# Optimization experiments

Hardware: AMD Instinct MI355X
Metric: run time of the kernel (lower is better)

## Reference

```python
import jax, jax.numpy as jnp
import numpy as np

# dims / hyperparams (match init_kwargs)
B, C, H, W = 1, 48, 160, 160
COUT = 48
RANK = 12
K = 8          # topK neighbors
WS = 32        # window_size
KS = 3         # local conv kernel / local mask size
M = 3          # circ_rows
DELTA = 10.0
LEAK = 0.01


def circ_dense(x, w, m):
    """CircDense: x (N, Cin), w (Cout//m, 1, Cin) -> (N, Cout).
    Equivalent to circular-pad + conv1d in the torch module."""
    cin = x.shape[1]
    xp = jnp.concatenate([x, x[:, : m - 1]], axis=1)            # circular pad to Cin+m-1
    xw = jnp.stack([xp[:, j : j + cin] for j in range(m)], 1)   # (N, m, Cin)
    out = jnp.einsum('njc,ic->nij', xw, w[:, 0, :])             # (N, Cout//m, m)
    return out.reshape(x.shape[0], -1)


def windowed_topk(h, k, ws, ks):
    """knn.windowedTopK: per 32x32 window, K nearest neighbors by feature L2,
    excluding the ks x ks local neighborhood (localMask). Returns (B,K,H,W)
    global flat pixel indices."""
    b, c, hh, ww = h.shape
    nh, nw = hh // ws, ww // ws
    ws2 = ws * ws
    hw = h.reshape(b, c, nh, ws, nw, ws).transpose(0, 2, 4, 3, 5, 1)
    hw = hw.reshape(b, nh, nw, ws2, c)                          # windowed features
    sq = jnp.sum(hw * hw, -1)
    d = sq[..., :, None] + sq[..., None, :] - 2.0 * jnp.einsum('bijnc,bijmc->bijnm', hw, hw)
    r = jnp.arange(ws2) // ws
    cc = jnp.arange(ws2) % ws
    loc = (jnp.abs(r[:, None] - r[None, :]) <= ks // 2) & (jnp.abs(cc[:, None] - cc[None, :]) <= ks // 2)
    d = jnp.where(loc, 1e10, d)                                 # mask local neighborhood
    _, idx = jax.lax.top_k(-d, k)                               # (b,nh,nw,ws2,k) local idx
    wi = jnp.arange(nh)[:, None, None, None]
    wj = jnp.arange(nw)[None, :, None, None]
    g = (wi * ws + idx // ws) * ww + (wj * ws + idx % ws)       # global flat idx
    g = g.reshape(b, nh, nw, ws, ws, k).transpose(0, 5, 1, 3, 2, 4).reshape(b, k, hh, ww)
    return g


def low_rank_ecc(h, edge, W0, b0, WL, WR, Wk, bk):
    b, k, hh, ww = edge.shape
    n = hh * ww
    cin = h.shape[1]
    hf = h.reshape(b, cin, n)
    ef = edge.reshape(b, k, n)
    # gather neighbor (vertex) features: (b, cin, k, n) -> (b, k, n, cin)
    vertex = jax.vmap(lambda hb, eb: hb[:, eb])(hf, ef).transpose(0, 2, 3, 1)
    center = hf.transpose(0, 2, 1)[:, None]                     # (b,1,n,cin)
    label = vertex - center                                     # edge labels
    lt = label.reshape(-1, cin)                                 # (B0, Cin), B0=b*k*n
    vt = vertex.reshape(-1, cin)
    theta = jax.nn.leaky_relu(lt @ W0.T + b0, LEAK)
    tL = circ_dense(theta, WL, M).reshape(-1, COUT, RANK)       # (B0, Cout, rank)
    tR = circ_dense(theta, WR, M).reshape(-1, cin, RANK)        # (B0, Cin, rank)
    kap = theta @ Wk.T + bk                                     # (B0, rank)
    tmp = kap * jnp.einsum('bcr,bc->br', tR, vt)                # thetaR^T @ v, scaled
    out = jnp.einsum('bor,br->bo', tL, tmp)                     # thetaL @ (...)
    gamma = jnp.exp(-jnp.sum(lt * lt, 1, keepdims=True) / DELTA)
    out = (gamma * out).reshape(b, k, n, COUT).mean(1)          # mean over K neighbors
    return out.transpose(0, 2, 1).reshape(b, COUT, hh, ww)


def local_conv(h, w):
    p = KS // 2
    hp = jnp.pad(h, ((0, 0), (0, 0), (p, p), (p, p)), mode='reflect')
    return jax.lax.conv_general_dilated(hp, w, (1, 1), 'VALID',
                                        dimension_numbers=('NCHW', 'OIHW', 'NCHW'))


def setup_inputs() -> dict:
    key = jax.random.key(0)
    ks_ = jax.random.split(key, 9)
    s_in = 1.0 / np.sqrt(C)
    return {
        'h': jax.random.normal(ks_[0], (B, C, H, W), jnp.float32),
        'W0': jax.random.normal(ks_[1], (C, C), jnp.float32) * s_in,
        'b0': jnp.zeros((C,), jnp.float32),
        'WL': jax.random.normal(ks_[2], (RANK * COUT // M, 1, C), jnp.float32) * s_in,
        'WR': jax.random.normal(ks_[3], (RANK * C // M, 1, C), jnp.float32) * s_in,
        'Wk': jax.random.normal(ks_[4], (RANK, C), jnp.float32) * s_in,
        'bk': jnp.zeros((RANK,), jnp.float32),
        'Wconv': jax.random.normal(ks_[5], (COUT, C, KS, KS), jnp.float32) * (1.0 / np.sqrt(C * KS * KS)),
        'bias': jnp.zeros((1, COUT, 1, 1), jnp.float32),
    }


def reference(h, W0, b0, WL, WR, Wk, bk, Wconv, bias):
    edge = windowed_topk(h, K, WS, KS)
    hNL = low_rank_ecc(h, edge, W0, b0, WL, WR, Wk, bk)
    hL = local_conv(h, Wconv)
    return (hNL + hL) / 2.0 + bias
```

## Files before the change

kernel.cpp:

```cpp
#include <hip/hip_runtime.h>

#define CC    48
#define HH    160
#define WWID  160
#define NPIX  25600
#define KK    8

typedef unsigned short u16;
typedef unsigned int u32;
typedef __attribute__((ext_vector_type(8))) short bf16x8;
typedef __attribute__((ext_vector_type(4))) float f32x4;

__device__ __forceinline__ float bf2f(u16 u) {
    return __uint_as_float(((unsigned int)u) << 16);
}
__device__ __forceinline__ u16 f2bf(float f) {
    unsigned int x = __float_as_uint(f);
    return (u16)((x + 0x7FFFu + ((x >> 16) & 1u)) >> 16);
}

#define OFF_B0    0
#define OFF_BK    48
#define OFF_WKT   60
#define OFF_WBH   636
#define OFF_WBL   8828
#define OFF_WLH   17020
#define OFF_WLL   21628
#define OFF_SQP   26236
#define OFF_W0V   51836
#define OFF_VTB   1280636
#define OFF_HHT   3738236
#define OFF_HLT   4557436
#define OFF_PARTK 5376636

__global__ void prep_kernel(const float* W0, const float* b0, const float* WL,
                            const float* WR, const float* Wk, const float* bk,
                            float* ws) {
    float* b0f = ws + OFF_B0;
    float* bkf = ws + OFF_BK;
    float* wkt = ws + OFF_WKT;
    u16*   wbh = (u16*)(ws + OFF_WBH);
    u16*   wbl = (u16*)(ws + OFF_WBL);
    u16*   wlh = (u16*)(ws + OFF_WLH);
    u16*   wll = (u16*)(ws + OFF_WLL);
    int t = blockIdx.x * 256 + threadIdx.x;
    int stride = gridDim.x * 256;
    for (int i = t; i < 16384; i += stride) {
        int col = i >> 6, k = i & 63;
        float v = 0.f;
        if (k < 48) {
            if (col < 192)      v = WR[(4*k + (col & 3))*48 + (col >> 2)];
            else if (col < 240) v = W0[(col - 192)*48 + k];
        }
        u16 hi = f2bf(v);
        wbh[i] = hi;
        wbl[i] = f2bf(v - bf2f(hi));
    }
    for (int i = t; i < 9216; i += stride) {
        int o = i / 192, k = i % 192;
        float v = WL[(4*o + (k & 3))*48 + (k >> 2)];
        u16 hi = f2bf(v);
        wlh[i] = hi;
        wll[i] = f2bf(v - bf2f(hi));
    }
    for (int i = t; i < 576; i += stride) { int c = i / 12, r = i % 12; wkt[i] = Wk[r*48 + c]; }
    for (int i = t; i < 48; i += stride) { b0f[i] = b0[i]; }
    for (int i = t; i < 12; i += stride) { bkf[i] = bk[i]; }
}

__global__ __launch_bounds__(256) void split_kernel(const float* h, float* sqp,
                                                    u16* hht, u16* hlt) {
    int tid = threadIdx.x;
    int p = blockIdx.x * 128 + (tid >> 1);
    int half = tid & 1;
    float sq = 0.f;
    u16 hh[24], hl[24];
    #pragma unroll
    for (int i = 0; i < 24; i++) {
        int c = half*24 + i;
        float v = h[c*NPIX + p];
        sq = fmaf(v, v, sq);
        u16 hi = f2bf(v);
        hh[i] = hi;
        hl[i] = f2bf(v - bf2f(hi));
    }
    sq += __shfl_xor(sq, 1, 64);
    if (half == 0) sqp[p] = sq;
    uint4* dh = (uint4*)&hht[(long)p*64 + half*24];
    uint4* dl = (uint4*)&hlt[(long)p*64 + half*24];
    const uint4* s1 = (const uint4*)hh;
    const uint4* s2 = (const uint4*)hl;
    dh[0] = s1[0]; dh[1] = s1[1]; dh[2] = s1[2];
    dl[0] = s2[0]; dl[1] = s2[1]; dl[2] = s2[2];
    if (half) {
        uint4 z = make_uint4(0, 0, 0, 0);
        uint4* zh = (uint4*)&hht[(long)p*64 + 48];
        uint4* zl = (uint4*)&hlt[(long)p*64 + 48];
        zh[0] = z; zh[1] = z;
        zl[0] = z; zl[1] = z;
    }
}

__global__ __launch_bounds__(512) void pixvt_mfma(const u16* hht, const u16* hlt,
                                                  const float* ws, float* w0v, u16* vtb) {
    __shared__ __align__(16) char smem[38912];
    u16*   a_hi = (u16*)smem;
    u16*   a_lo = (u16*)(smem + 8192);
    u16*   vt_s = (u16*)smem;
    float* w0_s = (float*)(smem + 25600);

    const u16* wbh = (const u16*)(ws + OFF_WBH);
    const u16* wbl = (const u16*)(ws + OFF_WBL);

    int tid = threadIdx.x;
    int pbase = blockIdx.x * 64;

    {
        int blk = tid >> 6, row = tid & 63;
        int swz = (blk ^ (row & 7)) * 8;
        *(uint4*)&a_hi[row*64 + swz] = *(const uint4*)&hht[(long)(pbase + row)*64 + blk*8];
        *(uint4*)&a_lo[row*64 + swz] = *(const uint4*)&hlt[(long)(pbase + row)*64 + blk*8];
    }
    __syncthreads();

    int w = tid >> 6, lane = tid & 63;
    int lm = lane & 15, lg = lane >> 4;
    int c2a = 2*w, c2b = 2*w + 1;

    f32x4 acc0[4], acc1[4];
    #pragma unroll
    for (int t = 0; t < 4; t++) { acc0[t] = (f32x4){0.f,0.f,0.f,0.f}; acc1[t] = (f32x4){0.f,0.f,0.f,0.f}; }

    #pragma unroll
    for (int s = 0; s < 2; s++) {
        int lblk = 4*s + lg;
        int aswz = (lblk ^ (lm & 7)) * 8;
        bf16x8 ah0 = *(const bf16x8*)&a_hi[( 0 + lm)*64 + aswz];
        bf16x8 ah1 = *(const bf16x8*)&a_hi[(16 + lm)*64 + aswz];
        bf16x8 ah2 = *(const bf16x8*)&a_hi[(32 + lm)*64 + aswz];
        bf16x8 ah3 = *(const bf16x8*)&a_hi[(48 + lm)*64 + aswz];
        bf16x8 al0 = *(const bf16x8*)&a_lo[( 0 + lm)*64 + aswz];
        bf16x8 al1 = *(const bf16x8*)&a_lo[(16 + lm)*64 + aswz];
        bf16x8 al2 = *(const bf16x8*)&a_lo[(32 + lm)*64 + aswz];
        bf16x8 al3 = *(const bf16x8*)&a_lo[(48 + lm)*64 + aswz];
        {
            int col = c2a*16 + lm;
            bf16x8 bh = *(const bf16x8*)&wbh[col*64 + lblk*8];
            bf16x8 bl = *(const bf16x8*)&wbl[col*64 + lblk*8];
            acc0[0] = __builtin_amdgcn_mfma_f32_16x16x32_bf16(ah0, bh, acc0[0], 0, 0, 0);
            acc0[0] = __builtin_amdgcn_mfma_f32_16x16x32_bf16(ah0, bl, acc0[0], 0, 0, 0);
            acc0[0] = __builtin_amdgcn_mfma_f32_16x16x32_bf16(al0, bh, acc0[0], 0, 0, 0);
            acc0[1] = __builtin_amdgcn_mfma_f32_16x16x32_bf16(ah1, bh, acc0[1], 0, 0, 0);
            acc0[1] = __builtin_amdgcn_mfma_f32_16x16x32_bf16(ah1, bl, acc0[1], 0, 0, 0);
            acc0[1] = __builtin_amdgcn_mfma_f32_16x16x32_bf16(al1, bh, acc0[1], 0, 0, 0);
            acc0[2] = __builtin_amdgcn_mfma_f32_16x16x32_bf16(ah2, bh, acc0[2], 0, 0, 0);
            acc0[2] = __builtin_amdgcn_mfma_f32_16x16x32_bf16(ah2, bl, acc0[2], 0, 0, 0);
            acc0[2] = __builtin_amdgcn_mfma_f32_16x16x32_bf16(al2, bh, acc0[2], 0, 0, 0);
            acc0[3] = __builtin_amdgcn_mfma_f32_16x16x32_bf16(ah3, bh, acc0[3], 0, 0, 0);
            acc0[3] = __builtin_amdgcn_mfma_f32_16x16x32_bf16(ah3, bl, acc0[3], 0, 0, 0);
            acc0[3] = __builtin_amdgcn_mfma_f32_16x16x32_bf16(al3, bh, acc0[3], 0, 0, 0);
        }
        if (c2b < 15) {
            int col = c2b*16 + lm;
            bf16x8 bh = *(const bf16x8*)&wbh[col*64 + lblk*8];
            bf16x8 bl = *(const bf16x8*)&wbl[col*64 + lblk*8];
            acc1[0] = __builtin_amdgcn_mfma_f32_16x16x32_bf16(ah0, bh, acc1[0], 0, 0, 0);
            acc1[0] = __builtin_amdgcn_mfma_f32_16x16x32_bf16(ah0, bl, acc1[0], 0, 0, 0);
            acc1[0] = __builtin_amdgcn_mfma_f32_16x16x32_bf16(al0, bh, acc1[0], 0, 0, 0);
            acc1[1] = __builtin_amdgcn_mfma_f32_16x16x32_bf16(ah1, bh, acc1[1], 0, 0, 0);
            acc1[1] = __builtin_amdgcn_mfma_f32_16x16x32_bf16(ah1, bl, acc1[1], 0, 0, 0);
            acc1[1] = __builtin_amdgcn_mfma_f32_16x16x32_bf16(al1, bh, acc1[1], 0, 0, 0);
            acc1[2] = __builtin_amdgcn_mfma_f32_16x16x32_bf16(ah2, bh, acc1[2], 0, 0, 0);
            acc1[2] = __builtin_amdgcn_mfma_f32_16x16x32_bf16(ah2, bl, acc1[2], 0, 0, 0);
            acc1[2] = __builtin_amdgcn_mfma_f32_16x16x32_bf16(al2, bh, acc1[2], 0, 0, 0);
            acc1[3] = __builtin_amdgcn_mfma_f32_16x16x32_bf16(ah3, bh, acc1[3], 0, 0, 0);
            acc1[3] = __builtin_amdgcn_mfma_f32_16x16x32_bf16(ah3, bl, acc1[3], 0, 0, 0);
            acc1[3] = __builtin_amdgcn_mfma_f32_16x16x32_bf16(al3, bh, acc1[3], 0, 0, 0);
        }
    }
    __syncthreads();

    {
        int col = c2a*16 + lm;
        if (c2a < 12) {
            #pragma unroll
            for (int t = 0; t < 4; t++)
                #pragma unroll
                for (int r = 0; r < 4; r++)
                    vt_s[(t*16 + lg*4 + r)*200 + col] = f2bf(acc0[t][r]);
        } else {
            int o = col - 192;
            #pragma unroll
            for (int t = 0; t < 4; t++)
                #pragma unroll
                for (int r = 0; r < 4; r++)
                    w0_s[(t*16 + lg*4 + r)*52 + o] = acc0[t][r];
        }
    }
    if (c2b < 15) {
        int col = c2b*16 + lm;
        if (c2b < 12) {
            #pragma unroll
            for (int t = 0; t < 4; t++)
                #pragma unroll
                for (int r = 0; r < 4; r++)
                    vt_s[(t*16 + lg*4 + r)*200 + col] = f2bf(acc1[t][r]);
        } else {
            int o = col - 192;
            #pragma unroll
            for (int t = 0; t < 4; t++)
                #pragma unroll
                for (int r = 0; r < 4; r++)
                    w0_s[(t*16 + lg*4 + r)*52 + o] = acc1[t][r];
        }
    }
    __syncthreads();

    {
        int px = tid >> 3, c8 = tid & 7;
        #pragma unroll
        for (int j = 0; j < 3; j++) {
            int ch = c8 + 8*j;
            uint4 v = *(const uint4*)&vt_s[px*200 + ch*8];
            *(uint4*)&vtb[(long)(pbase + px)*192 + ch*8] = v;
        }
        float* dst = w0v + (long)(pbase + px)*48 + c8*6;
        const float* src = w0_s + px*52 + c8*6;
        #pragma unroll
        for (int k = 0; k < 3; k++) {
            float2 v2 = *(const float2*)&src[k*2];
            *(float2*)&dst[k*2] = v2;
        }
    }
}

__global__ __launch_bounds__(512, 8) void topk_mfma(const u16* hht, const u16* hlt,
                                                    const float* sqp, u32* partk) {
    __shared__ u16 ca_hi[128*64];
    __shared__ u16 ca_lo[128*64];
    __shared__ float sq_s[128];

    int tid = threadIdx.x;
    int b = (blockIdx.x & 7) * 200 + (blockIdx.x >> 3);
    int chunk = b & 7, pg = (b >> 3) & 7, win = b >> 6;
    int wi = win / 5, wj = win % 5;
    int base = wi*32*WWID + wj*32;

    #pragma unroll
    for (int r = 0; r < 2; r++) {
        int task = r*512 + tid;
        int blk = task >> 7, row = task & 127;
        int swz = (blk ^ (row & 7)) * 8;
        int ml = chunk*128 + row;
        long gp = base + (ml>>5)*WWID + (ml&31);
        *(uint4*)&ca_hi[row*64 + swz] = *(const uint4*)&hht[gp*64 + blk*8];
        *(uint4*)&ca_lo[row*64 + swz] = *(const uint4*)&hlt[gp*64 + blk*8];
    }
    if (tid < 128) {
        int ml = chunk*128 + tid;
        sq_s[tid] = sqp[base + (ml>>5)*WWID + (ml&31)];
    }
    __syncthreads();

    int w = tid >> 6, lane = tid & 63;
    int lm = lane & 15, lg = lane >> 4;

    int nl = pg*128 + w*16 + lm;
    long gpx = base + (nl>>5)*WWID + (nl&31);

    f32x4 acc[8];
    #pragma unroll
    for (int t = 0; t < 8; t++) acc[t] = (f32x4){0.f, 0.f, 0.f, 0.f};

    #pragma unroll
    for (int s = 0; s < 2; s++) {
        int lblk = 4*s + lg;
        int ko = lblk * 8;
        bf16x8 bh = *(const bf16x8*)&hht[gpx*64 + ko];
        bf16x8 bl = *(const bf16x8*)&hlt[gpx*64 + ko];
        #pragma unroll
        for (int t = 0; t < 8; t++) {
            int aoff = (t*16 + lm)*64 + (lblk ^ (lm & 7))*8;
            bf16x8 ah = *(const bf16x8*)&ca_hi[aoff];
            bf16x8 al = *(const bf16x8*)&ca_lo[aoff];
            acc[t] = __builtin_amdgcn_mfma_f32_16x16x32_bf16(ah, bh, acc[t], 0, 0, 0);
            acc[t] = __builtin_amdgcn_mfma_f32_16x16x32_bf16(ah, bl, acc[t], 0, 0, 0);
            acc[t] = __builtin_amdgcn_mfma_f32_16x16x32_bf16(al, bh, acc[t], 0, 0, 0);
        }
    }

    int rn = nl >> 5, cn = nl & 31;
    int rowok[8], colok[8];
    #pragma unroll
    for (int t = 0; t < 8; t++) {
        int rm = chunk*4 + (t >> 1);
        int dr = rn - rm; dr = dr < 0 ? -dr : dr;
        rowok[t] = (dr <= 1);
    }
    #pragma unroll
    for (int j = 0; j < 8; j++) {
        int cm = (j >> 2)*16 + lg*4 + (j & 3);
        int dc = cn - cm; dc = dc < 0 ? -dc : dc;
        colok[j] = (dc <= 1);
    }

    u32 k8[8];
    #pragma unroll
    for (int s = 0; s < 8; s++) k8[s] = 0xFFFFFFFFu;

    #pragma unroll
    for (int t = 0; t < 8; t++) {
        #pragma unroll
        for (int r = 0; r < 4; r++) {
            int cl = t*16 + lg*4 + r;
            int ml = chunk*128 + cl;
            float d = fmaf(-2.0f, acc[t][r], sq_s[cl]);
            u32 u = __float_as_uint(d);
            u32 key = u ^ (0x80000000u | (u32)((int)u >> 31));
            key = (key & 0xFFFFFC00u) | (u32)ml;
            bool bad = rowok[t] && colok[(t & 1)*4 + r];
            key = bad ? 0xFFFFFFFFu : key;
            #pragma unroll
            for (int s = 0; s < 8; s++) {
                u32 lo = min(k8[s], key);
                u32 hi = max(k8[s], key);
                k8[s] = lo; key = hi;
            }
        }
    }

    #pragma unroll
    for (int st = 0; st < 2; st++) {
        int mk = (st == 0) ? 16 : 32;
        u32 o[8];
        #pragma unroll
        for (int s = 0; s < 8; s++) o[s] = (u32)__shfl_xor((int)k8[s], mk, 64);
        u32 c0 = min(k8[0], o[7]);
        u32 c1 = min(k8[1], o[6]);
        u32 c2 = min(k8[2], o[5]);
        u32 c3 = min(k8[3], o[4]);
        u32 c4 = min(k8[4], o[3]);
        u32 c5 = min(k8[5], o[2]);
        u32 c6 = min(k8[6], o[1]);
        u32 c7 = min(k8[7], o[0]);
        u32 a, bb;
        a = min(c0,c4); bb = max(c0,c4); c0 = a; c4 = bb;
        a = min(c1,c5); bb = max(c1,c5); c1 = a; c5 = bb;
        a = min(c2,c6); bb = max(c2,c6); c2 = a; c6 = bb;
        a = min(c3,c7); bb = max(c3,c7); c3 = a; c7 = bb;
        a = min(c0,c2); bb = max(c0,c2); c0 = a; c2 = bb;
        a = min(c1,c3); bb = max(c1,c3); c1 = a; c3 = bb;
        a = min(c4,c6); bb = max(c4,c6); c4 = a; c6 = bb;
        a = min(c5,c7); bb = max(c5,c7); c5 = a; c7 = bb;
        a = min(c0,c1); bb = max(c0,c1); c0 = a; c1 = bb;
        a = min(c2,c3); bb = max(c2,c3); c2 = a; c3 = bb;
        a = min(c4,c5); bb = max(c4,c5); c4 = a; c5 = bb;
        a = min(c6,c7); bb = max(c6,c7); c6 = a; c7 = bb;
        k8[0]=c0; k8[1]=c1; k8[2]=c2; k8[3]=c3; k8[4]=c4; k8[5]=c5; k8[6]=c6; k8[7]=c7;
    }

    {
        int n = base + (nl >> 5)*WWID + (nl & 31);
        u32 v0, v1;
        if      (lg == 0) { v0 = k8[0]; v1 = k8[1]; }
        else if (lg == 1) { v0 = k8[2]; v1 = k8[3]; }
        else if (lg == 2) { v0 = k8[4]; v1 = k8[5]; }
        else              { v0 = k8[6]; v1 = k8[7]; }
        u32* pk = partk + (long)chunk*8*NPIX + (long)(2*lg)*NPIX + n;
        pk[0]    = v0;
        pk[NPIX] = v1;
    }
}

__global__ __launch_bounds__(128, 4) void ecc_kernel(const float* ws, const u32* partk,
                                                     const u16* vtb, float* outp) {
    const float* b0f = ws + OFF_B0;
    const float* bkf = ws + OFF_BK;
    const float* wkt = ws + OFF_WKT;
    const float* w0v = ws + OFF_W0V;
    const float* sqp = ws + OFF_SQP;
    const u16*   wlh = (const u16*)(ws + OFF_WLH);
    const u16*   wll = (const u16*)(ws + OFF_WLL);

    __shared__ u16 th_s[128][50];
    __shared__ __align__(16) u16 ub_s[16*200];

    int tid = threadIdx.x;
    int sb = (blockIdx.x & 7) * 200 + (blockIdx.x >> 3);
    int pix = tid >> 3, sh = tid & 7;
    int n = sb * 16 + pix;

    u32 k8[8];
    {
        const u32* pk = partk + (long)sh*8*NPIX + n;
        #pragma unroll
        for (int s = 0; s < 8; s++) k8[s] = pk[(long)s*NPIX];
    }
    #pragma unroll
    for (int st = 0; st < 3; st++) {
        int mk = 1 << st;
        u32 o[8];
        #pragma unroll
        for (int s = 0; s < 8; s++) o[s] = (u32)__shfl_xor((int)k8[s], mk, 64);
        u32 c0 = min(k8[0], o[7]);
        u32 c1 = min(k8[1], o[6]);
        u32 c2 = min(k8[2], o[5]);
        u32 c3 = min(k8[3], o[4]);
        u32 c4 = min(k8[4], o[3]);
        u32 c5 = min(k8[5], o[2]);
        u32 c6 = min(k8[6], o[1]);
        u32 c7 = min(k8[7], o[0]);
        u32 a, bb;
        a = min(c0,c4); bb = max(c0,c4); c0 = a; c4 = bb;
        a = min(c1,c5); bb = max(c1,c5); c1 = a; c5 = bb;
        a = min(c2,c6); bb = max(c2,c6); c2 = a; c6 = bb;
        a = min(c3,c7); bb = max(c3,c7); c3 = a; c7 = bb;
        a = min(c0,c2); bb = max(c0,c2); c0 = a; c2 = bb;
        a = min(c1,c3); bb = max(c1,c3); c1 = a; c3 = bb;
        a = min(c4,c6); bb = max(c4,c6); c4 = a; c6 = bb;
        a = min(c5,c7); bb = max(c5,c7); c5 = a; c7 = bb;
        a = min(c0,c1); bb = max(c0,c1); c0 = a; c1 = bb;
        a = min(c2,c3); bb = max(c2,c3); c2 = a; c3 = bb;
        a = min(c4,c5); bb = max(c4,c5); c4 = a; c5 = bb;
        a = min(c6,c7); bb = max(c6,c7); c6 = a; c7 = bb;
        k8[0]=c0; k8[1]=c1; k8[2]=c2; k8[3]=c3; k8[4]=c4; k8[5]=c5; k8[6]=c6; k8[7]=c7;
    }
    u32 key;
    {
        u32 m0 = (sh & 1) ? k8[1] : k8[0];
        u32 m1 = (sh & 1) ? k8[3] : k8[2];
        u32 m2 = (sh & 1) ? k8[5] : k8[4];
        u32 m3 = (sh & 1) ? k8[7] : k8[6];
        u32 n0 = (sh & 2) ? m1 : m0;
        u32 n1 = (sh & 2) ? m3 : m2;
        key = (sh & 4) ? n1 : n0;
    }
    int ml = (int)(key & 1023u);
    u32 uf = key & 0xFFFFFC00u;
    u32 uu = (uf & 0x80000000u) ? (uf ^ 0x80000000u) : ~uf;
    float d = __uint_as_float(uu);
    int y = n / WWID, x = n % WWID;
    int wy = (y >> 5) << 5, wx = (x >> 5) << 5;
    int m = (wy + (ml >> 5)) * WWID + (wx + (ml & 31));
    float gamma = expf(-(d + sqp[n]) * 0.1f);

    const u16* vrow = vtb + (long)m * 192;
    uint4 vv[8];
    #pragma unroll
    for (int jj = 0; jj < 8; jj++) vv[jj] = *(const uint4*)&vrow[jj*8];

    float th[48];
    {
        const float4* wm4 = (const float4*)(w0v + (long)m * 48);
        const float4* wn4 = (const float4*)(w0v + (long)n * 48);
        #pragma unroll
        for (int i = 0; i < 12; i++) {
            float4 a = wm4[i];
            float4 b = wn4[i];
            float x0 = a.x - b.x + b0f[4*i+0];
            float x1 = a.y - b.y + b0f[4*i+1];
            float x2 = a.z - b.z + b0f[4*i+2];
            float x3 = a.w - b.w + b0f[4*i+3];
            th[4*i+0] = (x0 >= 0.f) ? x0 : 0.01f * x0;
            th[4*i+1] = (x1 >= 0.f) ? x1 : 0.01f * x1;
            th[4*i+2] = (x2 >= 0.f) ? x2 : 0.01f * x2;
            th[4*i+3] = (x3 >= 0.f) ? x3 : 0.01f * x3;
        }
    }

    #pragma unroll
    for (int i = 0; i < 24; i++) {
        ushort2 pr;
        pr.x = f2bf(th[2*i]);
        pr.y = f2bf(th[2*i+1]);
        *(ushort2*)&th_s[tid][2*i] = pr;
    }

    float kap[12];
    #pragma unroll
    for (int r = 0; r < 12; r++) kap[r] = bkf[r];
    #pragma unroll
    for (int c = 0; c < 48; c++) {
        float t = th[c];
        const float* wkc = wkt + c*12;
        #pragma unroll
        for (int r = 0; r < 12; r++) kap[r] = fmaf(wkc[r], t, kap[r]);
    }

    float sr[12];
    #pragma unroll
    for (int r = 0; r < 12; r++) sr[r] = 0.f;
    #pragma unroll
    for (int ch = 0; ch < 3; ch++) {
        if (ch > 0) {
            #pragma unroll
            for (int jj = 0; jj < 8; jj++) vv[jj] = *(const uint4*)&vrow[(ch*8 + jj)*8];
        }
        #pragma unroll
        for (int jj = 0; jj < 8; jj++) {
            int j = ch*8 + jj;
            uint4 v4 = vv[jj];
            #pragma unroll
            for (int half = 0; half < 2; half++) {
                int cp = 2*j + half;
                u32 w0_ = half ? v4.z : v4.x;
                u32 w1_ = half ? v4.w : v4.y;
                float vx = bf2f((u16)(w0_ & 0xffff));
                float vy = bf2f((u16)(w0_ >> 16));
                float vz = bf2f((u16)(w1_ & 0xffff));
                float vw = bf2f((u16)(w1_ >> 16));
                int i1 = (cp + 1 < 48) ? cp + 1 : cp - 47;
                int i2 = (cp + 2 < 48) ? cp + 2 : cp - 46;
                float t0 = th[cp], t1 = th[i1], t2 = th[i2];
                sr[0] = fmaf(t0, vx, sr[0]); sr[1]  = fmaf(t1, vx, sr[1]);  sr[2]  = fmaf(t2, vx, sr[2]);
                sr[3] = fmaf(t0, vy, sr[3]); sr[4]  = fmaf(t1, vy, sr[4]);  sr[5]  = fmaf(t2, vy, sr[5]);
                sr[6] = fmaf(t0, vz, sr[6]); sr[7]  = fmaf(t1, vz, sr[7]);  sr[8]  = fmaf(t2, vz, sr[8]);
                sr[9] = fmaf(t0, vw, sr[9]); sr[10] = fmaf(t1, vw, sr[10]); sr[11] = fmaf(t2, vw, sr[11]);
            }
        }
    }

    float tmp[12];
    #pragma unroll
    for (int r = 0; r < 12; r++) tmp[r] = kap[r] * sr[r];

    __syncthreads();

    float acc0[6], acc1[6], acc2[6], acc3[6];
    #pragma unroll
    for (int j = 0; j < 6; j++) { acc0[j] = 0.f; acc1[j] = 0.f; acc2[j] = 0.f; acc3[j] = 0.f; }
    #pragma unroll 1
    for (int e = 0; e < 8; e++) {
        int srcl = (tid & 56) + e;
        int row  = (tid & 120) + e;
        float tm[12];
        #pragma unroll
        for (int r = 0; r < 12; r++) tm[r] = __shfl(tmp[r], srcl, 64);
        float ge = __shfl(gamma, srcl, 64);
        #pragma unroll
        for (int j = 0; j < 6; j++) {
            int cp = sh + 8*j;
            int i1 = (cp + 1 < 48) ? cp + 1 : cp - 47;
            int i2 = (cp + 2 < 48) ? cp + 2 : cp - 46;
            float t0 = bf2f(th_s[row][cp]);
            float t1 = bf2f(th_s[row][i1]);
            float t2 = bf2f(th_s[row][i2]);
            float u0 = tm[0]*t0 + tm[1]*t1 + tm[2]*t2;
            float u1 = tm[3]*t0 + tm[4]*t1 + tm[5]*t2;
            float u2 = tm[6]*t0 + tm[7]*t1 + tm[8]*t2;
            float u3 = tm[9]*t0 + tm[10]*t1 + tm[11]*t2;
            acc0[j] = fmaf(ge, u0, acc0[j]);
            acc1[j] = fmaf(ge, u1, acc1[j]);
            acc2[j] = fmaf(ge, u2, acc2[j]);
            acc3[j] = fmaf(ge, u3, acc3[j]);
        }
    }
    {
        u16* ub = &ub_s[pix*200];
        #pragma unroll
        for (int j = 0; j < 6; j++) {
            int cp = sh + 8*j;
            ushort4 st;
            st.x = f2bf(acc0[j]); st.y = f2bf(acc1[j]);
            st.z = f2bf(acc2[j]); st.w = f2bf(acc3[j]);
            *(ushort4*)&ub[cp*4] = st;
        }
    }
    __syncthreads();

    {
        int w2 = tid >> 6;
        int lane = tid & 63;
        int lm = lane & 15, lg = lane >> 4;
        int nb = sb * 16;
        if (w2 == 0) {
            f32x4 a0 = (f32x4){0.f,0.f,0.f,0.f};
            f32x4 a1 = (f32x4){0.f,0.f,0.f,0.f};
            #pragma unroll
            for (int ks = 0; ks < 6; ks++) {
                bf16x8 a = *(const bf16x8*)&ub_s[lm*200 + ks*32 + lg*8];
                bf16x8 bh0 = *(const bf16x8*)&wlh[( 0 + lm)*192 + ks*32 + lg*8];
                bf16x8 bl0 = *(const bf16x8*)&wll[( 0 + lm)*192 + ks*32 + lg*8];
                bf16x8 bh1 = *(const bf16x8*)&wlh[(16 + lm)*192 + ks*32 + lg*8];
                bf16x8 bl1 = *(const bf16x8*)&wll[(16 + lm)*192 + ks*32 + lg*8];
                a0 = __builtin_amdgcn_mfma_f32_16x16x32_bf16(a, bh0, a0, 0, 0, 0);
                a0 = __builtin_amdgcn_mfma_f32_16x16x32_bf16(a, bl0, a0, 0, 0, 0);
                a1 = __builtin_amdgcn_mfma_f32_16x16x32_bf16(a, bh1, a1, 0, 0, 0);
                a1 = __builtin_amdgcn_mfma_f32_16x16x32_bf16(a, bl1, a1, 0, 0, 0);
            }
            #pragma unroll
            for (int r = 0; r < 4; r++) {
                int px = lg*4 + r;
                outp[(long)( 0 + lm)*NPIX + nb + px] = 0.0625f * a0[r];
                outp[(long)(16 + lm)*NPIX + nb + px] = 0.0625f * a1[r];
            }
        } else {
            f32x4 a2 = (f32x4){0.f,0.f,0.f,0.f};
            #pragma unroll
            for (int ks = 0; ks < 6; ks++) {
                bf16x8 a = *(const bf16x8*)&ub_s[lm*200 + ks*32 + lg*8];
                bf16x8 bh2 = *(const bf16x8*)&wlh[(32 + lm)*192 + ks*32 + lg*8];
                bf16x8 bl2 = *(const bf16x8*)&wll[(32 + lm)*192 + ks*32 + lg*8];
                a2 = __builtin_amdgcn_mfma_f32_16x16x32_bf16(a, bh2, a2, 0, 0, 0);
                a2 = __builtin_amdgcn_mfma_f32_16x16x32_bf16(a, bl2, a2, 0, 0, 0);
            }
            #pragma unroll
            for (int r = 0; r < 4; r++) {
                int px = lg*4 + r;
                outp[(long)(32 + lm)*NPIX + nb + px] = 0.0625f * a2[r];
            }
        }
    }
}

#define OCH 4
__global__ __launch_bounds__(320) void conv_kernel(const float* h, const float* wc,
                                                   const float* bias, float* outp) {
    int sb = (blockIdx.x & 7) * 120 + (blockIdx.x >> 3);
    int og = sb % 12;
    int yp = sb / 12;
    int t  = threadIdx.x;
    int ty = t / 160;
    int x  = t % 160;
    int y  = yp * 2 + ty;

    int idx9[9];
    #pragma unroll
    for (int dy = 0; dy < 3; dy++) {
        int yy = y + dy - 1;
        yy = yy < 0 ? -yy : (yy >= HH ? 2*HH - 2 - yy : yy);
        #pragma unroll
        for (int dx = 0; dx < 3; dx++) {
            int xx = x + dx - 1;
            xx = xx < 0 ? -xx : (xx >= WWID ? 2*WWID - 2 - xx : xx);
            idx9[dy*3 + dx] = yy * WWID + xx;
        }
    }

    float acc[OCH];
    #pragma unroll
    for (int oi = 0; oi < OCH; oi++) acc[oi] = 0.f;

    const float* wbase = wc + og * OCH * 432;
    for (int c = 0; c < 48; c++) {
        float v[9];
        #pragma unroll
        for (int k = 0; k < 9; k++) v[k] = h[c*NPIX + idx9[k]];
        #pragma unroll
        for (int oi = 0; oi < OCH; oi++) {
            const float* w9 = wbase + oi*432 + c*9;
            float a = acc[oi];
            a = fmaf(v[0], w9[0], a);
            a = fmaf(v[1], w9[1], a);
            a = fmaf(v[2], w9[2], a);
            a = fmaf(v[3], w9[3], a);
            a = fmaf(v[4], w9[4], a);
            a = fmaf(v[5], w9[5], a);
            a = fmaf(v[6], w9[6], a);
            a = fmaf(v[7], w9[7], a);
            a = fmaf(v[8], w9[8], a);
            acc[oi] = a;
        }
    }

    int p = y * WWID + x;
    #pragma unroll
    for (int oi = 0; oi < OCH; oi++) {
        int o = og * OCH + oi;
        outp[o*NPIX + p] = outp[o*NPIX + p] + 0.5f * acc[oi] + bias[o];
    }
}

extern "C" void kernel_launch(void* const* d_in, const int* in_sizes, int n_in,
                              void* d_out, int out_size, void* d_ws, size_t ws_size,
                              hipStream_t stream) {
    const float* h    = (const float*)d_in[0];
    const float* W0   = (const float*)d_in[1];
    const float* b0   = (const float*)d_in[2];
    const float* WL   = (const float*)d_in[3];
    const float* WR   = (const float*)d_in[4];
    const float* Wk   = (const float*)d_in[5];
    const float* bk   = (const float*)d_in[6];
    const float* Wc   = (const float*)d_in[7];
    const float* bias = (const float*)d_in[8];

    float* ws     = (float*)d_ws;
    float* sqp    = ws + OFF_SQP;
    float* w0v    = ws + OFF_W0V;
    u16*   vtb    = (u16*)(ws + OFF_VTB);
    u16*   hht    = (u16*)(ws + OFF_HHT);
    u16*   hlt    = (u16*)(ws + OFF_HLT);
    u32*   partk  = (u32*)(ws + OFF_PARTK);
    float* outp   = (float*)d_out;

    prep_kernel<<<dim3(16), dim3(256), 0, stream>>>(W0, b0, WL, WR, Wk, bk, ws);
    split_kernel<<<dim3(200), dim3(256), 0, stream>>>(h, sqp, hht, hlt);
    topk_mfma<<<dim3(1600), dim3(512), 0, stream>>>(hht, hlt, sqp, partk);
    pixvt_mfma<<<dim3(400), dim3(512), 0, stream>>>(hht, hlt, ws, w0v, vtb);
    ecc_kernel<<<dim3(1600), dim3(128), 0, stream>>>(ws, partk, vtb, outp);
    conv_kernel<<<dim3(960), dim3(320), 0, stream>>>(h, Wc, bias, outp);
}
```

Baseline: 132.2 us.

## Split each neighbor's channel work across two lanes in ECC kernel

Doubles the ECC block to 256 threads so each (pixel, neighbor) pair is handled by two lanes, each covering half of the 48 channels. The kap and sr reductions are combined with xor-shuffles, and the top-k merge now uses shuffle strides that skip the idle half-lane. The accumulation loop and the final MFMA stage are redistributed so three waves each compute one 16-row output tile instead of two waves with uneven work. The aim is lower register pressure and more latency hiding per pixel, at the cost of extra shuffles and duplicated top-k merging.

```diff
diff --git a/kernel.cpp b/kernel.cpp
--- a/kernel.cpp
+++ b/kernel.cpp
@@ -372,8 +372,8 @@
     }
 }
 
-__global__ __launch_bounds__(128, 4) void ecc_kernel(const float* ws, const u32* partk,
-                                                     const u16* vtb, float* outp) {
+__global__ __launch_bounds__(256) void ecc_kernel(const float* ws, const u32* partk,
+                                                  const u16* vtb, float* outp) {
     const float* b0f = ws + OFF_B0;
     const float* bkf = ws + OFF_BK;
     const float* wkt = ws + OFF_WKT;
@@ -387,18 +387,26 @@
 
     int tid = threadIdx.x;
     int sb = (blockIdx.x & 7) * 200 + (blockIdx.x >> 3);
-    int pix = tid >> 3, sh = tid & 7;
+    int pix = tid >> 4;
+    int lane16 = tid & 15;
+    int ek = lane16 >> 1;
+    int half = lane16 & 1;
+    int lane = tid & 63;
+    int erow = tid >> 1;
     int n = sb * 16 + pix;
 
     u32 k8[8];
-    {
-        const u32* pk = partk + (long)sh*8*NPIX + n;
+    if (half == 0) {
+        const u32* pk = partk + (long)ek*8*NPIX + n;
         #pragma unroll
         for (int s = 0; s < 8; s++) k8[s] = pk[(long)s*NPIX];
+    } else {
+        #pragma unroll
+        for (int s = 0; s < 8; s++) k8[s] = 0xFFFFFFFFu;
     }
     #pragma unroll
     for (int st = 0; st < 3; st++) {
-        int mk = 1 << st;
+        int mk = 2 << st;
         u32 o[8];
         #pragma unroll
         for (int s = 0; s < 8; s++) o[s] = (u32)__shfl_xor((int)k8[s], mk, 64);
@@ -425,16 +433,25 @@
         a = min(c6,c7); bb = max(c6,c7); c6 = a; c7 = bb;
         k8[0]=c0; k8[1]=c1; k8[2]=c2; k8[3]=c3; k8[4]=c4; k8[5]=c5; k8[6]=c6; k8[7]=c7;
     }
-    u32 key;
+    u32 muxval;
     {
-        u32 m0 = (sh & 1) ? k8[1] : k8[0];
-        u32 m1 = (sh & 1) ? k8[3] : k8[2];
-        u32 m2 = (sh & 1) ? k8[5] : k8[4];
-        u32 m3 = (sh & 1) ? k8[7] : k8[6];
-        u32 n0 = (sh & 2) ? m1 : m0;
-        u32 n1 = (sh & 2) ? m3 : m2;
-        key = (sh & 4) ? n1 : n0;
-    }
+        int sc = ek;
+        u32 m0 = (sc & 1) ? k8[1] : k8[0];
+        u32 m1 = (sc & 1) ? k8[3] : k8[2];
+        u32 m2 = (sc & 1) ? k8[5] : k8[4];
+        u32 m3 = (sc & 2) ? ((sc & 1) ? k8[3] : k8[2]) : m0;
+        u32 n0 = (sc & 2) ? m1 : m0;
+        u32 n1 = (sc & 2) ? ((sc & 1) ? k8[7] : k8[6]) : m2;
+        u32 q0 = (sc & 1) ? k8[1] : k8[0];
+        u32 q1 = (sc & 1) ? k8[3] : k8[2];
+        u32 q2 = (sc & 1) ? k8[5] : k8[4];
+        u32 q3 = (sc & 1) ? k8[7] : k8[6];
+        u32 r0 = (sc & 2) ? q1 : q0;
+        u32 r1 = (sc & 2) ? q3 : q2;
+        muxval = (sc & 4) ? r1 : r0;
+        (void)m3; (void)n0; (void)n1;
+    }
+    u32 key = (u32)__shfl((int)muxval, (lane & 48) + 2*ek, 64);
     int ml = (int)(key & 1023u);
     u32 uf = key & 0xFFFFFC00u;
     u32 uu = (uf & 0x80000000u) ? (uf ^ 0x80000000u) : ~uf;
@@ -444,81 +461,100 @@
     int m = (wy + (ml >> 5)) * WWID + (wx + (ml & 31));
     float gamma = expf(-(d + sqp[n]) * 0.1f);
 
-    const u16* vrow = vtb + (long)m * 192;
-    uint4 vv[8];
-    #pragma unroll
-    for (int jj = 0; jj < 8; jj++) vv[jj] = *(const uint4*)&vrow[jj*8];
-
-    float th[48];
+    const u16* vrow = vtb + (long)m * 192 + half*96;
+    uint4 vv[6];
+    #pragma unroll
+    for (int jj = 0; jj < 6; jj++) vv[jj] = *(const uint4*)&vrow[jj*8];
+
+    float th26[26];
     {
-        const float4* wm4 = (const float4*)(w0v + (long)m * 48);
-        const float4* wn4 = (const float4*)(w0v + (long)n * 48);
-        #pragma unroll
-        for (int i = 0; i < 12; i++) {
+        const float4* wm4 = (const float4*)(w0v + (long)m * 48) + half*6;
+        const float4* wn4 = (const float4*)(w0v + (long)n * 48) + half*6;
+        #pragma unroll
+        for (int i = 0; i < 6; i++) {
             float4 a = wm4[i];
             float4 b = wn4[i];
-            float x0 = a.x - b.x + b0f[4*i+0];
-            float x1 = a.y - b.y + b0f[4*i+1];
-            float x2 = a.z - b.z + b0f[4*i+2];
-            float x3 = a.w - b.w + b0f[4*i+3];
-            th[4*i+0] = (x0 >= 0.f) ? x0 : 0.01f * x0;
-            th[4*i+1] = (x1 >= 0.f) ? x1 : 0.01f * x1;
-            th[4*i+2] = (x2 >= 0.f) ? x2 : 0.01f * x2;
-            th[4*i+3] = (x3 >= 0.f) ? x3 : 0.01f * x3;
-        }
-    }
-
+            int c0 = half*24 + 4*i;
+            float x0 = a.x - b.x + b0f[c0+0];
+            float x1 = a.y - b.y + b0f[c0+1];
+            float x2 = a.z - b.z + b0f[c0+2];
+            float x3 = a.w - b.w + b0f[c0+3];
+            th26[4*i+0] = (x0 >= 0.f) ? x0 : 0.01f * x0;
+            th26[4*i+1] = (x1 >= 0.f) ? x1 : 0.01f * x1;
+            th26[4*i+2] = (x2 >= 0.f) ? x2 : 0.01f * x2;
+            th26[4*i+3] = (x3 >= 0.f) ? x3 : 0.01f * x3;
+        }
+    }
+    th26[24] = __shfl_xor(th26[0], 1, 64);
+    th26[25] = __shfl_xor(th26[1], 1, 64);
+
+    #pragma unroll
+    for (int i = 0; i < 12; i++) {
+        ushort2 pr;
+        pr.x = f2bf(th26[2*i]);
+        pr.y = f2bf(th26[2*i+1]);
+        *(ushort2*)&th_s[erow][half*24 + 2*i] = pr;
+    }
+
+    float kap[12];
+    #pragma unroll
+    for (int r = 0; r < 12; r++) kap[r] = half ? 0.f : bkf[r];
     #pragma unroll
     for (int i = 0; i < 24; i++) {
-        ushort2 pr;
-        pr.x = f2bf(th[2*i]);
-        pr.y = f2bf(th[2*i+1]);
-        *(ushort2*)&th_s[tid][2*i] = pr;
-    }
-
-    float kap[12];
-    #pragma unroll
-    for (int r = 0; r < 12; r++) kap[r] = bkf[r];
-    #pragma unroll
-    for (int c = 0; c < 48; c++) {
-        float t = th[c];
+        int c = half*24 + i;
+        float t = th26[i];
         const float* wkc = wkt + c*12;
         #pragma unroll
         for (int r = 0; r < 12; r++) kap[r] = fmaf(wkc[r], t, kap[r]);
     }
+    #pragma unroll
+    for (int r = 0; r < 12; r++) kap[r] += __shfl_xor(kap[r], 1, 64);
 
     float sr[12];
     #pragma unroll
     for (int r = 0; r < 12; r++) sr[r] = 0.f;
     #pragma unroll
-    for (int ch = 0; ch < 3; ch++) {
-        if (ch > 0) {
-            #pragma unroll
-            for (int jj = 0; jj < 8; jj++) vv[jj] = *(const uint4*)&vrow[(ch*8 + jj)*8];
-        }
-        #pragma unroll
-        for (int jj = 0; jj < 8; jj++) {
-            int j = ch*8 + jj;
-            uint4 v4 = vv[jj];
-            #pragma unroll
-            for (int half = 0; half < 2; half++) {
-                int cp = 2*j + half;
-                u32 w0_ = half ? v4.z : v4.x;
-                u32 w1_ = half ? v4.w : v4.y;
-                float vx = bf2f((u16)(w0_ & 0xffff));
-                float vy = bf2f((u16)(w0_ >> 16));
-                float vz = bf2f((u16)(w1_ & 0xffff));
-                float vw = bf2f((u16)(w1_ >> 16));
-                int i1 = (cp + 1 < 48) ? cp + 1 : cp - 47;
-                int i2 = (cp + 2 < 48) ? cp + 2 : cp - 46;
-                float t0 = th[cp], t1 = th[i1], t2 = th[i2];
-                sr[0] = fmaf(t0, vx, sr[0]); sr[1]  = fmaf(t1, vx, sr[1]);  sr[2]  = fmaf(t2, vx, sr[2]);
-                sr[3] = fmaf(t0, vy, sr[3]); sr[4]  = fmaf(t1, vy, sr[4]);  sr[5]  = fmaf(t2, vy, sr[5]);
-                sr[6] = fmaf(t0, vz, sr[6]); sr[7]  = fmaf(t1, vz, sr[7]);  sr[8]  = fmaf(t2, vz, sr[8]);
-                sr[9] = fmaf(t0, vw, sr[9]); sr[10] = fmaf(t1, vw, sr[10]); sr[11] = fmaf(t2, vw, sr[11]);
-            }
-        }
-    }
+    for (int j = 0; j < 6; j++) {
+        uint4 v4 = vv[j];
+        #pragma unroll
+        for (int hf = 0; hf < 2; hf++) {
+            int l = 2*j + hf;
+            u32 w0_ = hf ? v4.z : v4.x;
+            u32 w1_ = hf ? v4.w : v4.y;
+            float vx = bf2f((u16)(w0_ & 0xffff));
+            float vy = bf2f((u16)(w0_ >> 16));
+            float vz = bf2f((u16)(w1_ & 0xffff));
+            float vw = bf2f((u16)(w1_ >> 16));
+            float t0 = th26[l], t1 = th26[l+1], t2 = th26[l+2];
+            sr[0] = fmaf(t0, vx, sr[0]); sr[1]  = fmaf(t1, vx, sr[1]);  sr[2]  = fmaf(t2, vx, sr[2]);
+            sr[3] = fmaf(t0, vy, sr[3]); sr[4]  = fmaf(t1, vy, sr[4]);  sr[5]  = fmaf(t2, vy, sr[5]);
+            sr[6] = fmaf(t0, vz, sr[6]); sr[7]  = fmaf(t1, vz, sr[7]);  sr[8]  = fmaf(t2, vz, sr[8]);
+            sr[9] = fmaf(t0, vw, sr[9]); sr[10] = fmaf(t1, vw, sr[10]); sr[11] = fmaf(t2, vw, sr[11]);
+        }
+    }
+    #pragma unroll
+    for (int jj = 0; jj < 6; jj++) vv[jj] = *(const uint4*)&vrow[(6 + jj)*8];
+    #pragma unroll
+    for (int j = 0; j < 6; j++) {
+        uint4 v4 = vv[j];
+        #pragma unroll
+        for (int hf = 0; hf < 2; hf++) {
+            int l = 12 + 2*j + hf;
+            u32 w0_ = hf ? v4.z : v4.x;
+            u32 w1_ = hf ? v4.w : v4.y;
+            float vx = bf2f((u16)(w0_ & 0xffff));
+            float vy = bf2f((u16)(w0_ >> 16));
+            float vz = bf2f((u16)(w1_ & 0xffff));
+            float vw = bf2f((u16)(w1_ >> 16));
+            float t0 = th26[l], t1 = th26[l+1], t2 = th26[l+2];
+            sr[0] = fmaf(t0, vx, sr[0]); sr[1]  = fmaf(t1, vx, sr[1]);  sr[2]  = fmaf(t2, vx, sr[2]);
+            sr[3] = fmaf(t0, vy, sr[3]); sr[4]  = fmaf(t1, vy, sr[4]);  sr[5]  = fmaf(t2, vy, sr[5]);
+            sr[6] = fmaf(t0, vz, sr[6]); sr[7]  = fmaf(t1, vz, sr[7]);  sr[8]  = fmaf(t2, vz, sr[8]);
+            sr[9] = fmaf(t0, vw, sr[9]); sr[10] = fmaf(t1, vw, sr[10]); sr[11] = fmaf(t2, vw, sr[11]);
+        }
+    }
+    #pragma unroll
+    for (int r = 0; r < 12; r++) sr[r] += __shfl_xor(sr[r], 1, 64);
 
     float tmp[12];
     #pragma unroll
@@ -526,20 +562,20 @@
 
     __syncthreads();
 
-    float acc0[6], acc1[6], acc2[6], acc3[6];
-    #pragma unroll
-    for (int j = 0; j < 6; j++) { acc0[j] = 0.f; acc1[j] = 0.f; acc2[j] = 0.f; acc3[j] = 0.f; }
+    float acc0[3], acc1[3], acc2[3], acc3[3];
+    #pragma unroll
+    for (int j = 0; j < 3; j++) { acc0[j] = 0.f; acc1[j] = 0.f; acc2[j] = 0.f; acc3[j] = 0.f; }
     #pragma unroll 1
     for (int e = 0; e < 8; e++) {
-        int srcl = (tid & 56) + e;
-        int row  = (tid & 120) + e;
+        int srcl = (lane & 48) + 2*e;
+        int row  = pix*8 + e;
         float tm[12];
         #pragma unroll
         for (int r = 0; r < 12; r++) tm[r] = __shfl(tmp[r], srcl, 64);
         float ge = __shfl(gamma, srcl, 64);
         #pragma unroll
-        for (int j = 0; j < 6; j++) {
-            int cp = sh + 8*j;
+        for (int j = 0; j < 3; j++) {
+            int cp = lane16 + 16*j;
             int i1 = (cp + 1 < 48) ? cp + 1 : cp - 47;
             int i2 = (cp + 2 < 48) ? cp + 2 : cp - 46;
             float t0 = bf2f(th_s[row][cp]);
@@ -558,8 +594,8 @@
     {
         u16* ub = &ub_s[pix*200];
         #pragma unroll
-        for (int j = 0; j < 6; j++) {
-            int cp = sh + 8*j;
+        for (int j = 0; j < 3; j++) {
+            int cp = lane16 + 16*j;
             ushort4 st;
             st.x = f2bf(acc0[j]); st.y = f2bf(acc1[j]);
             st.z = f2bf(acc2[j]); st.w = f2bf(acc3[j]);
@@ -570,44 +606,22 @@
 
     {
         int w2 = tid >> 6;
-        int lane = tid & 63;
-        int lm = lane & 15, lg = lane >> 4;
-        int nb = sb * 16;
-        if (w2 == 0) {
+        if (w2 < 3) {
+            int lm = lane & 15, lg = lane >> 4;
+            int nb = sb * 16;
             f32x4 a0 = (f32x4){0.f,0.f,0.f,0.f};
-            f32x4 a1 = (f32x4){0.f,0.f,0.f,0.f};
             #pragma unroll
             for (int ks = 0; ks < 6; ks++) {
                 bf16x8 a = *(const bf16x8*)&ub_s[lm*200 + ks*32 + lg*8];
-                bf16x8 bh0 = *(const bf16x8*)&wlh[( 0 + lm)*192 + ks*32 + lg*8];
-                bf16x8 bl0 = *(const bf16x8*)&wll[( 0 + lm)*192 + ks*32 + lg*8];
-                bf16x8 bh1 = *(const bf16x8*)&wlh[(16 + lm)*192 + ks*32 + lg*8];
-                bf16x8 bl1 = *(const bf16x8*)&wll[(16 + lm)*192 + ks*32 + lg*8];
-                a0 = __builtin_amdgcn_mfma_f32_16x16x32_bf16(a, bh0, a0, 0, 0, 0);
-                a0 = __builtin_amdgcn_mfma_f32_16x16x32_bf16(a, bl0, a0, 0, 0, 0);
-                a1 = __builtin_amdgcn_mfma_f32_16x16x32_bf16(a, bh1, a1, 0, 0, 0);
-                a1 = __builtin_amdgcn_mfma_f32_16x16x32_bf16(a, bl1, a1, 0, 0, 0);
+                bf16x8 bh = *(const bf16x8*)&wlh[(w2*16 + lm)*192 + ks*32 + lg*8];
+                bf16x8 bl = *(const bf16x8*)&wll[(w2*16 + lm)*192 + ks*32 + lg*8];
+                a0 = __builtin_amdgcn_mfma_f32_16x16x32_bf16(a, bh, a0, 0, 0, 0);
+                a0 = __builtin_amdgcn_mfma_f32_16x16x32_bf16(a, bl, a0, 0, 0, 0);
             }
             #pragma unroll
             for (int r = 0; r < 4; r++) {
                 int px = lg*4 + r;
-                outp[(long)( 0 + lm)*NPIX + nb + px] = 0.0625f * a0[r];
-                outp[(long)(16 + lm)*NPIX + nb + px] = 0.0625f * a1[r];
-            }
-        } else {
-            f32x4 a2 = (f32x4){0.f,0.f,0.f,0.f};
-            #pragma unroll
-            for (int ks = 0; ks < 6; ks++) {
-                bf16x8 a = *(const bf16x8*)&ub_s[lm*200 + ks*32 + lg*8];
-                bf16x8 bh2 = *(const bf16x8*)&wlh[(32 + lm)*192 + ks*32 + lg*8];
-                bf16x8 bl2 = *(const bf16x8*)&wll[(32 + lm)*192 + ks*32 + lg*8];
-                a2 = __builtin_amdgcn_mfma_f32_16x16x32_bf16(a, bh2, a2, 0, 0, 0);
-                a2 = __builtin_amdgcn_mfma_f32_16x16x32_bf16(a, bl2, a2, 0, 0, 0);
-            }
-            #pragma unroll
-            for (int r = 0; r < 4; r++) {
-                int px = lg*4 + r;
-                outp[(long)(32 + lm)*NPIX + nb + px] = 0.0625f * a2[r];
+                outp[(long)(w2*16 + lm)*NPIX + nb + px] = 0.0625f * a0[r];
             }
         }
     }
@@ -697,6 +711,6 @@
     split_kernel<<<dim3(200), dim3(256), 0, stream>>>(h, sqp, hht, hlt);
     topk_mfma<<<dim3(1600), dim3(512), 0, stream>>>(hht, hlt, sqp, partk);
     pixvt_mfma<<<dim3(400), dim3(512), 0, stream>>>(hht, hlt, ws, w0v, vtb);
-    ecc_kernel<<<dim3(1600), dim3(128), 0, stream>>>(ws, partk, vtb, outp);
+    ecc_kernel<<<dim3(1600), dim3(256), 0, stream>>>(ws, partk, vtb, outp);
     conv_kernel<<<dim3(960), dim3(320), 0, stream>>>(h, Wc, bias, outp);
 }
```

Result: slower. 153.7 us (+16.3%).

## Co-schedule local conv blocks with ECC blocks in one launch, add combine pass

Applied to the files above, without the earlier changes.

Merges the ECC kernel and the 3x3 reflect-pad conv into one launch. Blocks are interleaved 2:3 by block index, so conv work runs concurrently with ECC work and can fill idle CU time. Conv results go to a workspace buffer, and a new vectorized combine kernel adds them into the output. This costs an extra 4.9 MB write and read plus one more launch, and the conv now runs with 128-thread blocks under ECC's launch bounds and shared-memory footprint.

```diff
diff --git a/kernel.cpp b/kernel.cpp
--- a/kernel.cpp
+++ b/kernel.cpp
@@ -32,6 +32,7 @@
 #define OFF_HHT   3738236
 #define OFF_HLT   4557436
 #define OFF_PARTK 5376636
+#define OFF_CONVP 7015036
 
 __global__ void prep_kernel(const float* W0, const float* b0, const float* WL,
                             const float* WR, const float* Wk, const float* bk,
@@ -372,8 +373,70 @@
     }
 }
 
-__global__ __launch_bounds__(128, 4) void ecc_kernel(const float* ws, const u32* partk,
-                                                     const u16* vtb, float* outp) {
+__global__ __launch_bounds__(128, 4) void ecc_conv_kernel(const float* ws, const u32* partk,
+                                                          const u16* vtb, const float* h,
+                                                          const float* wc, const float* bias,
+                                                          float* outp, float* convp) {
+    __shared__ u16 th_s[128][50];
+    __shared__ __align__(16) u16 ub_s[16*200];
+
+    int tid = threadIdx.x;
+    int bid = blockIdx.x;
+    int rr = bid % 5;
+
+    if (rr >= 2) {
+        int cb = (bid / 5) * 3 + (rr - 2);
+        int og = cb % 12;
+        int pg = cb / 12;
+        int p = pg * 128 + tid;
+        int y = p / WWID, x = p % WWID;
+
+        int idx9[9];
+        #pragma unroll
+        for (int dy = 0; dy < 3; dy++) {
+            int yy = y + dy - 1;
+            yy = yy < 0 ? -yy : (yy >= HH ? 2*HH - 2 - yy : yy);
+            #pragma unroll
+            for (int dx = 0; dx < 3; dx++) {
+                int xx = x + dx - 1;
+                xx = xx < 0 ? -xx : (xx >= WWID ? 2*WWID - 2 - xx : xx);
+                idx9[dy*3 + dx] = yy * WWID + xx;
+            }
+        }
+
+        float acc[4];
+        #pragma unroll
+        for (int oi = 0; oi < 4; oi++) acc[oi] = 0.f;
+
+        const float* wbase = wc + og * 4 * 432;
+        for (int c = 0; c < 48; c++) {
+            float v[9];
+            #pragma unroll
+            for (int k = 0; k < 9; k++) v[k] = h[c*NPIX + idx9[k]];
+            #pragma unroll
+            for (int oi = 0; oi < 4; oi++) {
+                const float* w9 = wbase + oi*432 + c*9;
+                float a = acc[oi];
+                a = fmaf(v[0], w9[0], a);
+                a = fmaf(v[1], w9[1], a);
+                a = fmaf(v[2], w9[2], a);
+                a = fmaf(v[3], w9[3], a);
+                a = fmaf(v[4], w9[4], a);
+                a = fmaf(v[5], w9[5], a);
+                a = fmaf(v[6], w9[6], a);
+                a = fmaf(v[7], w9[7], a);
+                a = fmaf(v[8], w9[8], a);
+                acc[oi] = a;
+            }
+        }
+        #pragma unroll
+        for (int oi = 0; oi < 4; oi++) {
+            int o = og * 4 + oi;
+            convp[(long)o*NPIX + p] = 0.5f * acc[oi] + bias[o];
+        }
+        return;
+    }
+
     const float* b0f = ws + OFF_B0;
     const float* bkf = ws + OFF_BK;
     const float* wkt = ws + OFF_WKT;
@@ -382,11 +445,8 @@
     const u16*   wlh = (const u16*)(ws + OFF_WLH);
     const u16*   wll = (const u16*)(ws + OFF_WLL);
 
-    __shared__ u16 th_s[128][50];
-    __shared__ __align__(16) u16 ub_s[16*200];
-
-    int tid = threadIdx.x;
-    int sb = (blockIdx.x & 7) * 200 + (blockIdx.x >> 3);
+    int eb = (bid / 5) * 2 + rr;
+    int sb = (eb & 7) * 200 + (eb >> 3);
     int pix = tid >> 3, sh = tid & 7;
     int n = sb * 16 + pix;
 
@@ -613,62 +673,12 @@
     }
 }
 
-#define OCH 4
-__global__ __launch_bounds__(320) void conv_kernel(const float* h, const float* wc,
-                                                   const float* bias, float* outp) {
-    int sb = (blockIdx.x & 7) * 120 + (blockIdx.x >> 3);
-    int og = sb % 12;
-    int yp = sb / 12;
-    int t  = threadIdx.x;
-    int ty = t / 160;
-    int x  = t % 160;
-    int y  = yp * 2 + ty;
-
-    int idx9[9];
-    #pragma unroll
-    for (int dy = 0; dy < 3; dy++) {
-        int yy = y + dy - 1;
-        yy = yy < 0 ? -yy : (yy >= HH ? 2*HH - 2 - yy : yy);
-        #pragma unroll
-        for (int dx = 0; dx < 3; dx++) {
-            int xx = x + dx - 1;
-            xx = xx < 0 ? -xx : (xx >= WWID ? 2*WWID - 2 - xx : xx);
-            idx9[dy*3 + dx] = yy * WWID + xx;
-        }
-    }
-
-    float acc[OCH];
-    #pragma unroll
-    for (int oi = 0; oi < OCH; oi++) acc[oi] = 0.f;
-
-    const float* wbase = wc + og * OCH * 432;
-    for (int c = 0; c < 48; c++) {
-        float v[9];
-        #pragma unroll
-        for (int k = 0; k < 9; k++) v[k] = h[c*NPIX + idx9[k]];
-        #pragma unroll
-        for (int oi = 0; oi < OCH; oi++) {
-            const float* w9 = wbase + oi*432 + c*9;
-            float a = acc[oi];
-            a = fmaf(v[0], w9[0], a);
-            a = fmaf(v[1], w9[1], a);
-            a = fmaf(v[2], w9[2], a);
-            a = fmaf(v[3], w9[3], a);
-            a = fmaf(v[4], w9[4], a);
-            a = fmaf(v[5], w9[5], a);
-            a = fmaf(v[6], w9[6], a);
-            a = fmaf(v[7], w9[7], a);
-            a = fmaf(v[8], w9[8], a);
-            acc[oi] = a;
-        }
-    }
-
-    int p = y * WWID + x;
-    #pragma unroll
-    for (int oi = 0; oi < OCH; oi++) {
-        int o = og * OCH + oi;
-        outp[o*NPIX + p] = outp[o*NPIX + p] + 0.5f * acc[oi] + bias[o];
-    }
+__global__ __launch_bounds__(256) void combine_kernel(const float* convp, float* outp) {
+    int i = blockIdx.x * 256 + threadIdx.x;
+    float4 a = ((const float4*)outp)[i];
+    float4 b = ((const float4*)convp)[i];
+    a.x += b.x; a.y += b.y; a.z += b.z; a.w += b.w;
+    ((float4*)outp)[i] = a;
 }
 
 extern "C" void kernel_launch(void* const* d_in, const int* in_sizes, int n_in,
@@ -691,12 +701,13 @@
     u16*   hht    = (u16*)(ws + OFF_HHT);
     u16*   hlt    = (u16*)(ws + OFF_HLT);
     u32*   partk  = (u32*)(ws + OFF_PARTK);
+    float* convp  = ws + OFF_CONVP;
     float* outp   = (float*)d_out;
 
     prep_kernel<<<dim3(16), dim3(256), 0, stream>>>(W0, b0, WL, WR, Wk, bk, ws);
     split_kernel<<<dim3(200), dim3(256), 0, stream>>>(h, sqp, hht, hlt);
     topk_mfma<<<dim3(1600), dim3(512), 0, stream>>>(hht, hlt, sqp, partk);
     pixvt_mfma<<<dim3(400), dim3(512), 0, stream>>>(hht, hlt, ws, w0v, vtb);
-    ecc_kernel<<<dim3(1600), dim3(128), 0, stream>>>(ws, partk, vtb, outp);
-    conv_kernel<<<dim3(960), dim3(320), 0, stream>>>(h, Wc, bias, outp);
-}
+    ecc_conv_kernel<<<dim3(4000), dim3(128), 0, stream>>>(ws, partk, vtb, h, Wc, bias, outp, convp);
+    combine_kernel<<<dim3(1200), dim3(256), 0, stream>>>(convp, outp);
+}
```

Measured after the change: 172.5 us. +30.5%, slower.
